# Kernel optimization log

Hardware: AMD Instinct MI355X
Metric: run time of the kernel (lower is better)

## Reference

```python
import jax, jax.numpy as jnp
import numpy as np

N, K, H, W = 8, 16, 256, 256
C, P = 4, 100000


def setup_inputs() -> dict:
    key = jax.random.key(0)
    k1, k2, k3, k4, k5 = jax.random.split(key, 5)
    raw_idx = jax.random.randint(k1, (N, K, H, W), 0, P, dtype=jnp.int32)
    # per-pixel number of valid points in [0, K]; trailing slots are -1 (z-sorted convention)
    cnt = jax.random.randint(k2, (N, 1, H, W), 0, K + 1, dtype=jnp.int32)
    k_ar = jnp.arange(K, dtype=jnp.int32).reshape(1, K, 1, 1)
    fragments = jnp.where(k_ar < cnt, raw_idx, -1)
    alphas = jax.random.uniform(k3, (N, K, H, W), dtype=jnp.float32)
    ptclds = jax.random.uniform(k4, (C, P), dtype=jnp.float32)  # packed rgba features
    background_color = jax.random.uniform(k5, (3,), dtype=jnp.float32)
    return {"fragments": fragments, "alphas": alphas, "ptclds": ptclds,
            "background_color": background_color}


def reference(fragments, alphas, ptclds, background_color):
    # fragments: (N,K,H,W) int32, -1 = no point; alphas: (N,K,H,W); ptclds: (C,P)
    valid = fragments >= 0
    a = jnp.where(valid, alphas, jnp.zeros((), alphas.dtype))  # skipped points contribute 0
    # front-to-back transmittance: cum_k = prod_{j<k} (1 - a_j)  (exclusive cumprod)
    cum = jnp.cumprod(1.0 - a, axis=1)
    cum_excl = jnp.concatenate([jnp.ones_like(cum[:, :1]), cum[:, :-1]], axis=1)
    wts = a * cum_excl  # (N,K,H,W)
    idx = jnp.where(valid, fragments, 0)
    feats = ptclds.T[idx]  # gather -> (N,K,H,W,C)
    images = jnp.einsum('nkhw,nkhwc->nchw', wts, feats)  # (N,C,H,W)
    # background fill where no nearest point exists
    bg = jnp.concatenate([background_color, jnp.ones((1,), background_color.dtype)])  # rgba
    bg_mask = fragments[:, 0] < 0  # (N,H,W)
    images = jnp.where(bg_mask[:, None, :, :], bg[None, :, None, None], images)
    return images
```

## Files before the change

### kernel.cpp

```cpp
#include <hip/hip_runtime.h>

#define NB 8
#define KF 16
#define HGT 256
#define WID 256
#define HW (HGT * WID)
#define NPIX (NB * HW)
#define NPTS 100000
#define NCH 4

__global__ void ptclds_transpose_kernel(const float* __restrict__ pt,
                                        float4* __restrict__ ws) {
    int p = blockIdx.x * blockDim.x + threadIdx.x;
    if (p < NPTS) {
        ws[p] = make_float4(pt[p],
                            pt[NPTS + p],
                            pt[2 * NPTS + p],
                            pt[3 * NPTS + p]);
    }
}

template <bool PACKED>
__global__ __launch_bounds__(256, 6) void composite_kernel(
    const int* __restrict__ frags,
    const float* __restrict__ alphas,
    const float* __restrict__ pt,
    const float4* __restrict__ ws,
    const float* __restrict__ bg,
    float* __restrict__ out)
{
    int i = blockIdx.x * blockDim.x + threadIdx.x;
    if (i >= NPIX) return;

    int n  = i >> 16;
    int hw = i & (HW - 1);

    long base = (long)n * KF * HW + hw;

    int f[KF];
    float a[KF];
    #pragma unroll
    for (int k = 0; k < KF; ++k)
        f[k] = frags[base + (long)k * HW];
    #pragma unroll
    for (int k = 0; k < KF; ++k)
        a[k] = alphas[base + (long)k * HW];

    float4 acc = make_float4(0.f, 0.f, 0.f, 0.f);
    float T = 1.0f;

    #pragma unroll
    for (int k = 0; k < KF; ++k) {
        const bool v = f[k] >= 0;
        const int idx = v ? f[k] : 0;
        float4 g;
        if (PACKED) {
            g = ws[idx];
        } else {
            g = make_float4(pt[idx], pt[NPTS + idx],
                            pt[2 * NPTS + idx], pt[3 * NPTS + idx]);
        }
        const float av = v ? a[k] : 0.f;
        const float w = av * T;
        acc.x += w * g.x;
        acc.y += w * g.y;
        acc.z += w * g.z;
        acc.w += w * g.w;
        T *= (1.0f - av);
    }

    if (f[0] < 0) acc = make_float4(bg[0], bg[1], bg[2], 1.0f);

    long ob = (long)n * NCH * HW + hw;
    out[ob]          = acc.x;
    out[ob + HW]     = acc.y;
    out[ob + 2 * HW] = acc.z;
    out[ob + 3 * HW] = acc.w;
}

extern "C" void kernel_launch(void* const* d_in, const int* in_sizes, int n_in,
                              void* d_out, int out_size, void* d_ws, size_t ws_size,
                              hipStream_t stream) {
    const int*   frags  = (const int*)d_in[0];
    const float* alphas = (const float*)d_in[1];
    const float* pt     = (const float*)d_in[2];
    const float* bg     = (const float*)d_in[3];
    float* out = (float*)d_out;

    const bool packed = (ws_size >= (size_t)NPTS * sizeof(float4));

    if (packed) {
        float4* ws = (float4*)d_ws;
        ptclds_transpose_kernel<<<(NPTS + 255) / 256, 256, 0, stream>>>(pt, ws);
        composite_kernel<true><<<NPIX / 256, 256, 0, stream>>>(
            frags, alphas, pt, ws, bg, out);
    } else {
        composite_kernel<false><<<NPIX / 256, 256, 0, stream>>>(
            frags, alphas, pt, (const float4*)nullptr, bg, out);
    }
}
```

Measured before the change: 115.9 us.

## Split the K-depth compositing of each pixel across two threads

Each pixel's 16-point compositing is now split across two threads, each handling 8 depth slots. The back half's partial result is combined through shared memory, scaled by the front half's transmittance. This doubles the thread count and halves per-thread register pressure and serial gather latency, aiming for more memory-level parallelism on this bandwidth- and gather-bound kernel. In exchange it adds a block-wide barrier, shared-memory traffic, and leaves half the threads idle during the output write.

```diff
diff --git a/kernel.cpp b/kernel.cpp
--- a/kernel.cpp
+++ b/kernel.cpp
@@ -8,6 +8,7 @@
 #define NPIX (NB * HW)
 #define NPTS 100000
 #define NCH 4
+#define KHALF 8
 
 __global__ void ptclds_transpose_kernel(const float* __restrict__ pt,
                                         float4* __restrict__ ws) {
@@ -21,7 +22,7 @@
 }
 
 template <bool PACKED>
-__global__ __launch_bounds__(256, 6) void composite_kernel(
+__global__ __launch_bounds__(256, 6) void composite_split_kernel(
     const int* __restrict__ frags,
     const float* __restrict__ alphas,
     const float* __restrict__ pt,
@@ -29,30 +30,31 @@
     const float* __restrict__ bg,
     float* __restrict__ out)
 {
-    int i = blockIdx.x * blockDim.x + threadIdx.x;
-    if (i >= NPIX) return;
+    const int lpx  = threadIdx.x & 127;
+    const int half = threadIdx.x >> 7;
+    const int px   = (blockIdx.x << 7) | lpx;
 
-    int n  = i >> 16;
-    int hw = i & (HW - 1);
+    const int n  = px >> 16;
+    const int hw = px & (HW - 1);
 
-    long base = (long)n * KF * HW + hw;
+    long base = (long)n * KF * HW + (long)(half * KHALF) * HW + hw;
 
-    int f[KF];
-    float a[KF];
+    int f[KHALF];
+    float a[KHALF];
     #pragma unroll
-    for (int k = 0; k < KF; ++k)
-        f[k] = frags[base + (long)k * HW];
+    for (int j = 0; j < KHALF; ++j)
+        f[j] = frags[base + (long)j * HW];
     #pragma unroll
-    for (int k = 0; k < KF; ++k)
-        a[k] = alphas[base + (long)k * HW];
+    for (int j = 0; j < KHALF; ++j)
+        a[j] = alphas[base + (long)j * HW];
 
     float4 acc = make_float4(0.f, 0.f, 0.f, 0.f);
     float T = 1.0f;
 
     #pragma unroll
-    for (int k = 0; k < KF; ++k) {
-        const bool v = f[k] >= 0;
-        const int idx = v ? f[k] : 0;
+    for (int j = 0; j < KHALF; ++j) {
+        const bool v = f[j] >= 0;
+        const int idx = v ? f[j] : 0;
         float4 g;
         if (PACKED) {
             g = ws[idx];
@@ -60,7 +62,7 @@
             g = make_float4(pt[idx], pt[NPTS + idx],
                             pt[2 * NPTS + idx], pt[3 * NPTS + idx]);
         }
-        const float av = v ? a[k] : 0.f;
+        const float av = v ? a[j] : 0.f;
         const float w = av * T;
         acc.x += w * g.x;
         acc.y += w * g.y;
@@ -69,13 +71,24 @@
         T *= (1.0f - av);
     }
 
-    if (f[0] < 0) acc = make_float4(bg[0], bg[1], bg[2], 1.0f);
+    __shared__ float4 s_acc[128];
+    if (half == 1) s_acc[lpx] = acc;
+    __syncthreads();
 
-    long ob = (long)n * NCH * HW + hw;
-    out[ob]          = acc.x;
-    out[ob + HW]     = acc.y;
-    out[ob + 2 * HW] = acc.z;
-    out[ob + 3 * HW] = acc.w;
+    if (half == 0) {
+        const float4 acc1 = s_acc[lpx];
+        float4 r = make_float4(acc.x + T * acc1.x,
+                               acc.y + T * acc1.y,
+                               acc.z + T * acc1.z,
+                               acc.w + T * acc1.w);
+        if (f[0] < 0) r = make_float4(bg[0], bg[1], bg[2], 1.0f);
+
+        long ob = (long)n * NCH * HW + hw;
+        out[ob]          = r.x;
+        out[ob + HW]     = r.y;
+        out[ob + 2 * HW] = r.z;
+        out[ob + 3 * HW] = r.w;
+    }
 }
 
 extern "C" void kernel_launch(void* const* d_in, const int* in_sizes, int n_in,
@@ -88,14 +101,15 @@
     float* out = (float*)d_out;
 
     const bool packed = (ws_size >= (size_t)NPTS * sizeof(float4));
+    const int nblocks = (NPIX * 2) / 256;
 
     if (packed) {
         float4* ws = (float4*)d_ws;
         ptclds_transpose_kernel<<<(NPTS + 255) / 256, 256, 0, stream>>>(pt, ws);
-        composite_kernel<true><<<NPIX / 256, 256, 0, stream>>>(
+        composite_split_kernel<true><<<nblocks, 256, 0, stream>>>(
             frags, alphas, pt, ws, bg, out);
     } else {
-        composite_kernel<false><<<NPIX / 256, 256, 0, stream>>>(
+        composite_split_kernel<false><<<nblocks, 256, 0, stream>>>(
             frags, alphas, pt, (const float4*)nullptr, bg, out);
     }
 }
```

Measured after the change: 116.1 us. Within noise of the previous version (+0.2%).
